# Kernel optimization log

Hardware: AMD Instinct MI355X
Metric: run time of the kernel (lower is better)

Reference implementation:

```python
import jax, jax.numpy as jnp
import numpy as np

DIM = 384
HEADS = 12
HEAD_DIM = DIM // HEADS
WS = 7          # window_size
SS = 3          # shift_size (SW-MSA)
DIM_FF = 4 * DIM
EPS = 1e-5


def _rel_pos_index():
    coords = np.stack(np.meshgrid(np.arange(WS), np.arange(WS), indexing='ij'))
    cf = coords.reshape(2, -1)                       # (2, 49)
    rel = cf[:, :, None] - cf[:, None, :]            # (2, 49, 49)
    rel = rel.transpose(1, 2, 0).astype(np.int64)
    rel[:, :, 0] += WS - 1
    rel[:, :, 1] += WS - 1
    rel[:, :, 0] *= 2 * WS - 1
    return rel.sum(-1)                               # (49, 49)


def _attn_mask(Hp, Wp):
    # cyclic-shift mask, computed on static shapes with numpy
    img = np.zeros((Hp, Wp))
    slices = (slice(0, -WS), slice(-WS, -SS), slice(-SS, None))
    cnt = 0
    for hs in slices:
        for ws_ in slices:
            img[hs, ws_] = cnt
            cnt += 1
    mw = img.reshape(Hp // WS, WS, Wp // WS, WS).transpose(0, 2, 1, 3).reshape(-1, WS * WS)
    am = mw[:, None, :] - mw[:, :, None]             # unsqueeze(1) - unsqueeze(2)
    am = np.where(am != 0, -100.0, 0.0)
    return jnp.asarray(am, jnp.float32)              # (nW, 49, 49)


def _ln(x, g, b):
    mu = jnp.mean(x, -1, keepdims=True)
    var = jnp.mean(jnp.square(x - mu), -1, keepdims=True)
    return (x - mu) * jax.lax.rsqrt(var + EPS) * g + b


def setup_inputs() -> dict:
    key = jax.random.key(0)
    ks = jax.random.split(key, 8)
    B, H, W = 32, 56, 56
    s = 0.02
    return {
        'x': jax.random.normal(ks[0], (B, H * W, DIM), jnp.float32),
        'H': H, 'W': W,
        'rel_idx': jnp.asarray(_rel_pos_index(), jnp.int32),
        'rpb_table': jax.random.normal(ks[1], ((2 * WS - 1) ** 2, HEADS), jnp.float32) * s,
        'qkv_w': jax.random.normal(ks[2], (DIM, 3 * DIM), jnp.float32) * s,
        'proj_w': jax.random.normal(ks[3], (DIM, DIM), jnp.float32) * s,
        'proj_b': jnp.zeros((DIM,), jnp.float32),
        'norm1_g': jnp.ones((DIM,), jnp.float32),
        'norm1_b': jnp.zeros((DIM,), jnp.float32),
        'norm2_g': jnp.ones((DIM,), jnp.float32),
        'norm2_b': jnp.zeros((DIM,), jnp.float32),
        'ffn_w1': jax.random.normal(ks[4], (DIM, DIM_FF), jnp.float32) * s,
        'ffn_b1': jnp.zeros((DIM_FF,), jnp.float32),
        'ffn_w2': jax.random.normal(ks[5], (DIM_FF, DIM), jnp.float32) * s,
        'ffn_b2': jnp.zeros((DIM,), jnp.float32),
    }


def reference(x, H, W, rel_idx, rpb_table, qkv_w, proj_w, proj_b,
              norm1_g, norm1_b, norm2_g, norm2_b,
              ffn_w1, ffn_b1, ffn_w2, ffn_b2):
    B, L, C = x.shape
    shortcut = x
    h = _ln(x, norm1_g, norm1_b).reshape(B, H, W, C)

    pad_b = (WS - H % WS) % WS
    pad_r = (WS - W % WS) % WS
    if pad_b > 0 or pad_r > 0:
        h = jnp.pad(h, ((0, 0), (0, pad_b), (0, pad_r), (0, 0)))
    Hp, Wp = H + pad_b, W + pad_r

    if SS > 0:
        h = jnp.roll(h, (-SS, -SS), axis=(1, 2))

    # window partition -> (B*nW, 49, C)
    nHw, nWw = Hp // WS, Wp // WS
    win = h.reshape(B, nHw, WS, nWw, WS, C).transpose(0, 1, 3, 2, 4, 5)
    win = win.reshape(-1, WS * WS, C)
    Bw, N = win.shape[0], WS * WS

    # window attention
    qkv = (win @ qkv_w).reshape(Bw, N, 3, HEADS, HEAD_DIM)
    q, k, v = [qkv[:, :, i].transpose(0, 2, 1, 3) for i in range(3)]  # (Bw, heads, N, hd)
    attn = jnp.einsum('bhnd,bhmd->bhnm', q, k) / np.sqrt(HEAD_DIM)

    bias = rpb_table[rel_idx]                      # (N, N, heads)
    attn = attn + bias.transpose(2, 0, 1)[None]

    if SS > 0:
        mask = _attn_mask(Hp, Wp)                  # (nW, N, N)
        nW = mask.shape[0]
        attn = attn.reshape(B, nW, HEADS, N, N) + mask[None, :, None]
        attn = attn.reshape(Bw, HEADS, N, N)

    attn = jax.nn.softmax(attn, axis=-1)
    out = jnp.einsum('bhnm,bhmd->bnhd', attn, v).reshape(Bw, N, C)
    out = out @ proj_w + proj_b

    # window reverse
    out = out.reshape(B, nHw, nWw, WS, WS, C).transpose(0, 1, 3, 2, 4, 5)
    out = out.reshape(B, Hp, Wp, C)
    if SS > 0:
        out = jnp.roll(out, (SS, SS), axis=(1, 2))
    if pad_b > 0 or pad_r > 0:
        out = out[:, :H, :W, :]

    h = shortcut + out.reshape(B, H * W, C)
    ff = _ln(h, norm2_g, norm2_b)
    ff = jax.nn.gelu(ff @ ffn_w1 + ffn_b1, approximate=False) @ ffn_w2 + ffn_b2
    return h + ff
```

## Files before the change

### kernel.cpp

```cpp
#include <hip/hip_runtime.h>

#define DEV __device__ __forceinline__

typedef __bf16 bf16x8 __attribute__((ext_vector_type(8)));
typedef float  f32x4  __attribute__((ext_vector_type(4)));
typedef unsigned short u16x8 __attribute__((ext_vector_type(8)));
typedef unsigned short u16x4 __attribute__((ext_vector_type(4)));

DEV float b2f(unsigned short u) {
    unsigned int t = ((unsigned int)u) << 16;
    return __uint_as_float(t);
}
DEV unsigned short f2b(float f) {
    unsigned int u = __float_as_uint(f);
    unsigned int r = (u + 0x7FFFu + ((u >> 16) & 1u)) >> 16;
    return (unsigned short)r;
}
DEV unsigned char f2f8(float f) {
    return (unsigned char)(__builtin_amdgcn_cvt_pk_fp8_f32(f, f, 0, false) & 0xff);
}

DEV void gload_lds16(const void* g, void* l) {
    __builtin_amdgcn_global_load_lds(
        (const __attribute__((address_space(1))) void*)g,
        (__attribute__((address_space(3))) void*)l, 16, 0, 0);
}

DEV size_t win_to_tok(int row) {
    int w = row / 49, t = row - w * 49;
    int b  = w >> 6, widx = w & 63;
    int wi = widx >> 3, wj = widx & 7;
    int ti = t / 7, tj = t - ti * 7;
    int hh = wi * 7 + ti + 3; if (hh >= 56) hh -= 56;
    int ww = wj * 7 + tj + 3; if (ww >= 56) ww -= 56;
    return (size_t)b * 3136 + (size_t)hh * 56 + ww;
}

__global__ void wprep8(const float* __restrict__ src, unsigned char* __restrict__ dst,
                       int K, int N) {
    int idx = blockIdx.x * 256 + threadIdx.x;
    if (idx >= K * N) return;
    int k = idx / N, n = idx - k * N;
    dst[(size_t)n * K + k] = f2f8(src[idx]);
}

__global__ void btab_build(const int* __restrict__ rel_idx, const float* __restrict__ rpb,
                           float* __restrict__ tab) {
    int idx = blockIdx.x * 256 + threadIdx.x;
    if (idx >= 4 * 12 * 64 * 64) return;
    int col = idx & 63, row = (idx >> 6) & 63;
    int h = (idx >> 12) % 12, cls = idx / (12 * 4096);
    float v;
    if (row >= 49 || col >= 49) {
        v = -10000.f;
    } else {
        v = rpb[rel_idx[row * 49 + col] * 12 + h];
        int ti = row / 7, tj = row - (row / 7) * 7;
        int si = col / 7, sj = col - (col / 7) * 7;
        int lq = ((cls & 2) ? (ti < 4 ? 1 : 2) : 0) * 3 + ((cls & 1) ? (tj < 4 ? 1 : 2) : 0);
        int lk = ((cls & 2) ? (si < 4 ? 1 : 2) : 0) * 3 + ((cls & 1) ? (sj < 4 ? 1 : 2) : 0);
        if (lq != lk) v -= 100.f;
    }
    tab[idx] = v;
}

template <int REMAP>
__global__ __launch_bounds__(256) void ln_kernel(const float* __restrict__ x,
                                                 const float* __restrict__ g,
                                                 const float* __restrict__ b,
                                                 unsigned char* __restrict__ out,
                                                 int rows) {
    int r = blockIdx.x * 4 + (threadIdx.x >> 6);
    int lane = threadIdx.x & 63;
    if (r >= rows) return;
    size_t src = REMAP ? win_to_tok(r) : (size_t)r;
    const float* xp = x + src * 384;
    float v[6];
    float s = 0.f;
#pragma unroll
    for (int i = 0; i < 6; ++i) { v[i] = xp[i * 64 + lane]; s += v[i]; }
#pragma unroll
    for (int off = 32; off; off >>= 1) s += __shfl_xor(s, off, 64);
    float mu = s * (1.f / 384.f);
    float q = 0.f;
#pragma unroll
    for (int i = 0; i < 6; ++i) { float d = v[i] - mu; q += d * d; }
#pragma unroll
    for (int off = 32; off; off >>= 1) q += __shfl_xor(q, off, 64);
    float inv = rsqrtf(q * (1.f / 384.f) + 1e-5f);
    unsigned char* op = out + (size_t)r * 384;
#pragma unroll
    for (int i = 0; i < 6; ++i) {
        int c = i * 64 + lane;
        op[c] = f2f8((v[i] - mu) * inv * g[c] + b[c]);
    }
}

template <int MODE, int NBUF, int DEPTH, int SB, int MINW>
__global__ __launch_bounds__(256, MINW) void gemm_f8_kernel(const unsigned char* __restrict__ A,
                                                            const unsigned char* __restrict__ Bt,
                                                            int M, int N, int K,
                                                            const float* __restrict__ bias,
                                                            const float* __restrict__ resid,
                                                            unsigned char* __restrict__ outb8,
                                                            unsigned short* __restrict__ outb,
                                                            float* __restrict__ outf) {
    static_assert(SB ? (NBUF >= DEPTH + 2) : (NBUF >= DEPTH + 1), "ring too small");
    __shared__ unsigned char As[NBUF][128 * 64];
    __shared__ unsigned char Bs[NBUF][128 * 64];
    const int tid = threadIdx.x;
    const int wid = tid >> 6, lane = tid & 63;
    const int ntile = N >> 7;

    int bid = blockIdx.x;
    int nwg = gridDim.x;
    int swb = ((nwg & 7) == 0) ? ((bid & 7) * (nwg >> 3) + (bid >> 3)) : bid;
    const int mt = swb / ntile, nt = swb - mt * ntile;
    const int wr = wid >> 1, wc = wid & 1;

    f32x4 acc[4][4] = {};

    const int srow = tid >> 2;
    const unsigned char* Abase = A  + (size_t)(mt * 128) * K;
    const unsigned char* Bbase = Bt + (size_t)(nt * 128) * K;

    auto stage = [&](int buf, int k0) {
#pragma unroll
        for (int j = 0; j < 2; ++j) {
            int r  = j * 64 + srow;
            int gp = (tid & 3) ^ ((r >> 1) & 3);
            gload_lds16(Abase + (size_t)r * K + k0 + gp * 16, &As[buf][j * 4096 + tid * 16]);
            gload_lds16(Bbase + (size_t)r * K + k0 + gp * 16, &Bs[buf][j * 4096 + tid * 16]);
        }
    };

    const int fr = lane & 15, kq = lane >> 4;
    const int rowA = wr * 64 + fr;
    const int rowB = wc * 64 + fr;
    auto ldf8 = [&](const unsigned char* base, int row, int ks) -> long {
        int slot = ks * 4 + kq;
        int phys = ((((slot >> 1) ^ ((row >> 1) & 3)) << 1) | (slot & 1));
        return *(const long*)(base + row * 64 + phys * 8);
    };

    const int nk = K >> 6;
    stage(0, 0);
    if (DEPTH >= 2 && nk > 1) stage(1, 64);

    for (int t = 0; t < nk; ++t) {
        const int cur = t % NBUF;
        if (t + DEPTH < nk) {
            stage((t + DEPTH) % NBUF, (t + DEPTH) << 6);
            if constexpr (DEPTH == 1) {
                asm volatile("s_waitcnt vmcnt(4)" ::: "memory");
            } else {
                asm volatile("s_waitcnt vmcnt(8)" ::: "memory");
            }
        } else if (DEPTH >= 2 && t + 1 < nk) {
            asm volatile("s_waitcnt vmcnt(4)" ::: "memory");
        } else {
            asm volatile("s_waitcnt vmcnt(0)" ::: "memory");
        }
        __builtin_amdgcn_s_barrier();

        long a[4][2], b[4][2];
#pragma unroll
        for (int m = 0; m < 4; ++m) {
            a[m][0] = ldf8(As[cur], rowA + m * 16, 0);
            a[m][1] = ldf8(As[cur], rowA + m * 16, 1);
        }
#pragma unroll
        for (int n = 0; n < 4; ++n) {
            b[n][0] = ldf8(Bs[cur], rowB + n * 16, 0);
            b[n][1] = ldf8(Bs[cur], rowB + n * 16, 1);
        }
#pragma unroll
        for (int ks = 0; ks < 2; ++ks)
#pragma unroll
            for (int m = 0; m < 4; ++m)
#pragma unroll
                for (int n = 0; n < 4; ++n)
                    acc[m][n] = __builtin_amdgcn_mfma_f32_16x16x32_fp8_fp8(b[n][ks], a[m][ks], acc[m][n], 0, 0, 0);

        asm volatile("s_waitcnt lgkmcnt(0)" ::: "memory");
        if constexpr (SB == 0) __builtin_amdgcn_s_barrier();
    }

    const int row0 = mt * 128 + wr * 64;
    const int col0 = nt * 128 + wc * 64;
    const int rl = lane & 15;
    const int cq = (lane >> 4) << 2;
#pragma unroll
    for (int m = 0; m < 4; ++m) {
        int row = row0 + m * 16 + rl;
        size_t tok = 0;
        if constexpr (MODE == 1) tok = win_to_tok(row);
#pragma unroll
        for (int n = 0; n < 4; ++n) {
            int col = col0 + n * 16 + cq;
            f32x4 v = acc[m][n];
            if constexpr (MODE == 0) {
                u16x4 pk;
#pragma unroll
                for (int r = 0; r < 4; ++r) pk[r] = f2b(v[r]);
                *(u16x4*)&outb[(size_t)row * N + col] = pk;
            } else if constexpr (MODE == 1) {
                size_t o = tok * 384 + col;
                f32x4 rv = *(const f32x4*)&resid[o];
                f32x4 bb = *(const f32x4*)&bias[col];
                f32x4 ov = rv + v + bb;
                *(f32x4*)&outf[o] = ov;
            } else if constexpr (MODE == 2) {
                f32x4 bb = *(const f32x4*)&bias[col];
                float g4[4];
#pragma unroll
                for (int r = 0; r < 4; ++r) {
                    float t2 = v[r] + bb[r];
                    g4[r] = t2 / (1.f + __expf(-1.702f * t2));
                }
                int pk = 0;
                pk = __builtin_amdgcn_cvt_pk_fp8_f32(g4[0], g4[1], pk, false);
                pk = __builtin_amdgcn_cvt_pk_fp8_f32(g4[2], g4[3], pk, true);
                *(int*)(outb8 + (size_t)row * N + col) = pk;
            } else {
                size_t o = (size_t)row * N + col;
                f32x4 rv = *(const f32x4*)&resid[o];
                f32x4 bb = *(const f32x4*)&bias[col];
                f32x4 ov = rv + v + bb;
                *(f32x4*)&outf[o] = ov;
            }
        }
    }
}

__global__ __launch_bounds__(256, 2) void attn_kernel(const unsigned short* __restrict__ QKV,
                                                      const float* __restrict__ Btab,
                                                      unsigned char* __restrict__ O8) {
    __shared__ char lds[65536];
    char* Kl = lds;
    char* Vl = lds + 16384;
    char* Pl = lds + 32768;

    const int w   = blockIdx.x;
    const int tid = threadIdx.x, wid = tid >> 6, lane = tid & 63;
    const int fr  = lane & 15, kq = lane >> 4;
    const size_t base = (size_t)w * 49 * 1152;
    const int widx = w & 63, wi = widx >> 3, wj = widx & 7;
    const int cls = ((wi == 7) ? 2 : 0) | ((wj == 7) ? 1 : 0);
    const float* tb = Btab + (size_t)cls * 12 * 4096;
    constexpr float SCL = 0.17677669529663687f;

    for (int R = 0; R < 3; ++R) {
        if (R) __syncthreads();
        {
            f32x4 z = {};
#pragma unroll
            for (int j = 0; j < 8; ++j) *(f32x4*)(lds + j * 4096 + tid * 16) = z;
        }
        __syncthreads();
        {
            int hh = tid >> 6, h = R * 4 + hh;
#pragma unroll
            for (int it = 0; it < 4; ++it) {
                int i = (tid & 63) + it * 64;
                if (i < 196) {
                    int m = i >> 2, c = i & 3;
                    u16x8 kv = *(const u16x8*)&QKV[base + (size_t)m * 1152 + 384 + h * 32 + c * 8];
                    *(u16x8*)(Kl + hh * 4096 + m * 64 + (c ^ ((m >> 1) & 3)) * 16) = kv;
                    u16x8 vv = *(const u16x8*)&QKV[base + (size_t)m * 1152 + 768 + h * 32 + c * 8];
#pragma unroll
                    for (int j = 0; j < 8; ++j) {
                        int d = c * 8 + j;
                        *(unsigned short*)(Vl + hh * 4096 + d * 128 +
                                           (((m >> 3) ^ (d & 7)) * 16) + (m & 7) * 2) = vv[j];
                    }
                }
            }
        }
        __syncthreads();

        const int h = R * 4 + wid;
        const float* tbh = tb + h * 4096;

        bf16x8 aq[4], bk[4];
#pragma unroll
        for (int mi = 0; mi < 4; ++mi) {
            int row = mi * 16 + fr; if (row > 48) row = 48;
            aq[mi] = *(const bf16x8*)&QKV[base + (size_t)row * 1152 + h * 32 + kq * 8];
        }
#pragma unroll
        for (int ni = 0; ni < 4; ++ni) {
            int rk = ni * 16 + fr;
            bk[ni] = *(const bf16x8*)(Kl + wid * 4096 + rk * 64 + ((kq ^ ((rk >> 1) & 3)) * 16));
        }
        f32x4 s[4][4] = {};
#pragma unroll
        for (int mi = 0; mi < 4; ++mi)
#pragma unroll
            for (int ni = 0; ni < 4; ++ni)
                s[mi][ni] = __builtin_amdgcn_mfma_f32_16x16x32_bf16(bk[ni], aq[mi], s[mi][ni], 0, 0, 0);

        float linv_[4];
#pragma unroll
        for (int mi = 0; mi < 4; ++mi) {
            int row = mi * 16 + fr;
            const float* tr = tbh + row * 64 + kq * 4;
            f32x4 sv[4];
            float mx = -1e30f;
#pragma unroll
            for (int ni = 0; ni < 4; ++ni) {
                f32x4 bb = *(const f32x4*)&tr[ni * 16];
                sv[ni] = s[mi][ni] * SCL + bb;
                mx = fmaxf(mx, fmaxf(fmaxf(sv[ni][0], sv[ni][1]), fmaxf(sv[ni][2], sv[ni][3])));
            }
            mx = fmaxf(mx, __shfl_xor(mx, 16, 64));
            mx = fmaxf(mx, __shfl_xor(mx, 32, 64));
            float sm = 0.f;
#pragma unroll
            for (int ni = 0; ni < 4; ++ni)
#pragma unroll
                for (int r = 0; r < 4; ++r) { sv[ni][r] = __expf(sv[ni][r] - mx); sm += sv[ni][r]; }
            sm += __shfl_xor(sm, 16, 64);
            sm += __shfl_xor(sm, 32, 64);
            linv_[mi] = 1.f / sm;
#pragma unroll
            for (int ni = 0; ni < 4; ++ni) {
                int colb = ni * 16 + kq * 4;
                int phys = (colb >> 3) ^ (row & 7);
                u16x4 pk;
#pragma unroll
                for (int r = 0; r < 4; ++r) pk[r] = f2b(sv[ni][r]);
                *(u16x4*)(Pl + wid * 8192 + row * 128 + phys * 16 + (colb & 7) * 2) = pk;
            }
        }
        asm volatile("s_waitcnt lgkmcnt(0)" ::: "memory");
        __builtin_amdgcn_sched_barrier(0);

        f32x4 oacc[4][2] = {};
#pragma unroll
        for (int sl = 0; sl < 2; ++sl) {
            bf16x8 bv[2];
#pragma unroll
            for (int ni = 0; ni < 2; ++ni) {
                int d = ni * 16 + fr;
                bv[ni] = *(const bf16x8*)(Vl + wid * 4096 + d * 128 + (((sl * 4 + kq) ^ (d & 7)) * 16));
            }
#pragma unroll
            for (int mi = 0; mi < 4; ++mi) {
                int row = mi * 16 + fr;
                bf16x8 ap = *(const bf16x8*)(Pl + wid * 8192 + row * 128 + (((sl * 4 + kq) ^ (row & 7)) * 16));
#pragma unroll
                for (int ni = 0; ni < 2; ++ni)
                    oacc[mi][ni] = __builtin_amdgcn_mfma_f32_16x16x32_bf16(bv[ni], ap, oacc[mi][ni], 0, 0, 0);
            }
        }

#pragma unroll
        for (int mi = 0; mi < 4; ++mi) {
            int row = mi * 16 + fr;
            if (row < 49) {
                float li = linv_[mi];
                unsigned char* op = O8 + (size_t)(w * 49 + row) * 384 + h * 32 + kq * 4;
#pragma unroll
                for (int ni = 0; ni < 2; ++ni) {
                    int pk = 0;
                    pk = __builtin_amdgcn_cvt_pk_fp8_f32(oacc[mi][ni][0] * li, oacc[mi][ni][1] * li, pk, false);
                    pk = __builtin_amdgcn_cvt_pk_fp8_f32(oacc[mi][ni][2] * li, oacc[mi][ni][3] * li, pk, true);
                    *(int*)(op + ni * 16) = pk;
                }
            }
        }
    }
}

extern "C" void kernel_launch(void* const* d_in, const int* in_sizes, int n_in,
                              void* d_out, int out_size, void* d_ws, size_t ws_size,
                              hipStream_t stream) {
    const float* x     = (const float*)d_in[0];
    const int*   rel   = (const int*)  d_in[3];
    const float* rpb   = (const float*)d_in[4];
    const float* qkvw  = (const float*)d_in[5];
    const float* projw = (const float*)d_in[6];
    const float* projb = (const float*)d_in[7];
    const float* n1g   = (const float*)d_in[8];
    const float* n1b   = (const float*)d_in[9];
    const float* n2g   = (const float*)d_in[10];
    const float* n2b   = (const float*)d_in[11];
    const float* w1    = (const float*)d_in[12];
    const float* b1    = (const float*)d_in[13];
    const float* w2    = (const float*)d_in[14];
    const float* b2    = (const float*)d_in[15];
    float* out = (float*)d_out;

    const int T = in_sizes[0] / 384;

    char* ws = (char*)d_ws;
    size_t off = 0;
    auto alloc = [&](size_t bytes) {
        char* p = ws + off;
        off += (bytes + 255) & ~(size_t)255;
        return p;
    };
    unsigned char* Wq8  = (unsigned char*)alloc((size_t)1152 * 384);
    unsigned char* Wp8  = (unsigned char*)alloc((size_t)384 * 384);
    unsigned char* W18  = (unsigned char*)alloc((size_t)1536 * 384);
    unsigned char* W28  = (unsigned char*)alloc((size_t)384 * 1536);
    float*         Btab = (float*)       alloc((size_t)4 * 12 * 4096 * 4);
    unsigned char* slotA = (unsigned char*)alloc((size_t)T * 384);
    unsigned char* slotB = (unsigned char*)alloc((size_t)T * 1152 * 2);

    unsigned char*  X1  = slotA;
    unsigned char*  O8  = slotA;
    unsigned char*  X2  = slotA;
    unsigned short* QKV = (unsigned short*)slotB;
    unsigned char*  F8  = slotB;
    float*          Hh  = out;

    wprep8<<<dim3((1152 * 384 + 255) / 256), 256, 0, stream>>>(qkvw, Wq8, 384, 1152);
    wprep8<<<dim3((384 * 384 + 255) / 256),  256, 0, stream>>>(projw, Wp8, 384, 384);
    wprep8<<<dim3((384 * 1536 + 255) / 256), 256, 0, stream>>>(w1, W18, 384, 1536);
    wprep8<<<dim3((1536 * 384 + 255) / 256), 256, 0, stream>>>(w2, W28, 1536, 384);
    btab_build<<<dim3((4 * 12 * 4096 + 255) / 256), 256, 0, stream>>>(rel, rpb, Btab);

    ln_kernel<1><<<dim3(T / 4), 256, 0, stream>>>(x, n1g, n1b, X1, T);
    gemm_f8_kernel<0, 2, 1, 0, 4><<<dim3((T / 128) * (1152 / 128)), 256, 0, stream>>>(
        X1, Wq8, T, 1152, 384, nullptr, nullptr, nullptr, QKV, nullptr);
    attn_kernel<<<dim3(T / 49), 256, 0, stream>>>(QKV, Btab, O8);
    gemm_f8_kernel<1, 2, 1, 0, 4><<<dim3((T / 128) * (384 / 128)), 256, 0, stream>>>(
        O8, Wp8, T, 384, 384, projb, x, nullptr, nullptr, Hh);
    ln_kernel<0><<<dim3(T / 4), 256, 0, stream>>>(Hh, n2g, n2b, X2, T);
    gemm_f8_kernel<2, 2, 1, 0, 4><<<dim3((T / 128) * (1536 / 128)), 256, 0, stream>>>(
        X2, W18, T, 1536, 384, b1, nullptr, F8, nullptr, nullptr);
    gemm_f8_kernel<3, 4, 2, 1, 2><<<dim3((T / 128) * (384 / 128)), 256, 0, stream>>>(
        F8, W28, T, 384, 1536, b2, Hh, nullptr, nullptr, out);
}
```

Measured before the change: 696.2 us.

## Permute K layout of fp8 operands so GEMM fragments load as 16-byte reads

Applies a fixed permutation of the K index within each 64-element block to every producer of fp8 GEMM operands: weight prep, LayerNorm output, the GELU epilogue and the attention output. The GEMM inner loop can then fetch both k-steps of a fragment with one 16-byte LDS load per row instead of two 8-byte loads. This cuts the LDS instruction count in the hot loop, at the cost of byte-scattered writes in the producers and a layout contract shared across several kernels.

```diff
diff --git a/kernel.cpp b/kernel.cpp
--- a/kernel.cpp
+++ b/kernel.cpp
@@ -6,6 +6,7 @@
 typedef float  f32x4  __attribute__((ext_vector_type(4)));
 typedef unsigned short u16x8 __attribute__((ext_vector_type(8)));
 typedef unsigned short u16x4 __attribute__((ext_vector_type(4)));
+typedef long  longx2 __attribute__((ext_vector_type(2)));
 
 DEV float b2f(unsigned short u) {
     unsigned int t = ((unsigned int)u) << 16;
@@ -18,6 +19,11 @@
 }
 DEV unsigned char f2f8(float f) {
     return (unsigned char)(__builtin_amdgcn_cvt_pk_fp8_f32(f, f, 0, false) & 0xff);
+}
+
+DEV int kpos(int c) {
+    int s = (c >> 3) & 7;
+    return (c & ~63) | ((((s & 3) << 1) | (s >> 2)) << 3) | (c & 7);
 }
 
 DEV void gload_lds16(const void* g, void* l) {
@@ -41,7 +47,7 @@
     int idx = blockIdx.x * 256 + threadIdx.x;
     if (idx >= K * N) return;
     int k = idx / N, n = idx - k * N;
-    dst[(size_t)n * K + k] = f2f8(src[idx]);
+    dst[(size_t)n * K + kpos(k)] = f2f8(src[idx]);
 }
 
 __global__ void btab_build(const int* __restrict__ rel_idx, const float* __restrict__ rpb,
@@ -92,7 +98,7 @@
 #pragma unroll
     for (int i = 0; i < 6; ++i) {
         int c = i * 64 + lane;
-        op[c] = f2f8((v[i] - mu) * inv * g[c] + b[c]);
+        op[kpos(c)] = f2f8((v[i] - mu) * inv * g[c] + b[c]);
     }
 }
 
@@ -120,14 +126,13 @@
 
     f32x4 acc[4][4] = {};
 
-    const int srow = tid >> 2;
     const unsigned char* Abase = A  + (size_t)(mt * 128) * K;
     const unsigned char* Bbase = Bt + (size_t)(nt * 128) * K;
 
     auto stage = [&](int buf, int k0) {
 #pragma unroll
         for (int j = 0; j < 2; ++j) {
-            int r  = j * 64 + srow;
+            int r  = j * 64 + (tid >> 2);
             int gp = (tid & 3) ^ ((r >> 1) & 3);
             gload_lds16(Abase + (size_t)r * K + k0 + gp * 16, &As[buf][j * 4096 + tid * 16]);
             gload_lds16(Bbase + (size_t)r * K + k0 + gp * 16, &Bs[buf][j * 4096 + tid * 16]);
@@ -137,11 +142,7 @@
     const int fr = lane & 15, kq = lane >> 4;
     const int rowA = wr * 64 + fr;
     const int rowB = wc * 64 + fr;
-    auto ldf8 = [&](const unsigned char* base, int row, int ks) -> long {
-        int slot = ks * 4 + kq;
-        int phys = ((((slot >> 1) ^ ((row >> 1) & 3)) << 1) | (slot & 1));
-        return *(const long*)(base + row * 64 + phys * 8);
-    };
+    const int cb = (kq ^ ((fr >> 1) & 3)) << 4;
 
     const int nk = K >> 6;
     stage(0, 0);
@@ -163,17 +164,13 @@
         }
         __builtin_amdgcn_s_barrier();
 
-        long a[4][2], b[4][2];
-#pragma unroll
-        for (int m = 0; m < 4; ++m) {
-            a[m][0] = ldf8(As[cur], rowA + m * 16, 0);
-            a[m][1] = ldf8(As[cur], rowA + m * 16, 1);
-        }
-#pragma unroll
-        for (int n = 0; n < 4; ++n) {
-            b[n][0] = ldf8(Bs[cur], rowB + n * 16, 0);
-            b[n][1] = ldf8(Bs[cur], rowB + n * 16, 1);
-        }
+        longx2 a[4], b[4];
+#pragma unroll
+        for (int m = 0; m < 4; ++m)
+            a[m] = *(const longx2*)(&As[cur][(rowA + m * 16) * 64 + cb]);
+#pragma unroll
+        for (int n = 0; n < 4; ++n)
+            b[n] = *(const longx2*)(&Bs[cur][(rowB + n * 16) * 64 + cb]);
 #pragma unroll
         for (int ks = 0; ks < 2; ++ks)
 #pragma unroll
@@ -221,7 +218,7 @@
                 int pk = 0;
                 pk = __builtin_amdgcn_cvt_pk_fp8_f32(g4[0], g4[1], pk, false);
                 pk = __builtin_amdgcn_cvt_pk_fp8_f32(g4[2], g4[3], pk, true);
-                *(int*)(outb8 + (size_t)row * N + col) = pk;
+                *(int*)(outb8 + (size_t)row * N + kpos(col)) = pk;
             } else {
                 size_t o = (size_t)row * N + col;
                 f32x4 rv = *(const f32x4*)&resid[o];
@@ -360,13 +357,14 @@
             int row = mi * 16 + fr;
             if (row < 49) {
                 float li = linv_[mi];
-                unsigned char* op = O8 + (size_t)(w * 49 + row) * 384 + h * 32 + kq * 4;
+                unsigned char* opb = O8 + (size_t)(w * 49 + row) * 384;
 #pragma unroll
                 for (int ni = 0; ni < 2; ++ni) {
+                    int c = h * 32 + ni * 16 + kq * 4;
                     int pk = 0;
                     pk = __builtin_amdgcn_cvt_pk_fp8_f32(oacc[mi][ni][0] * li, oacc[mi][ni][1] * li, pk, false);
                     pk = __builtin_amdgcn_cvt_pk_fp8_f32(oacc[mi][ni][2] * li, oacc[mi][ni][3] * li, pk, true);
-                    *(int*)(op + ni * 16) = pk;
+                    *(int*)(opb + kpos(c)) = pk;
                 }
             }
         }
```

Result: faster. 678.9 us (-2.5%).
